# Kernel optimization log

Hardware: AMD Instinct MI355X
Metric: run time of the kernel (lower is better)

The kernel has to match this reference:

```python
import jax, jax.numpy as jnp
import numpy as np

DIM = 1024
N_OBJ = 2048
N_REL = 4096
H_CAT = 4
H_OUT = 6
OUT_CAT = DIM // 2            # 512, concat=True branch
OUT_NC = (DIM // 2) * H_OUT   # 3072, concat=False branch


def setup_inputs() -> dict:
    key = jax.random.key(0)
    ks = jax.random.split(key, 6)
    s = 0.02
    return {
        "feat_obj": jax.random.normal(ks[0], (N_OBJ, DIM), jnp.float32),
        "feat_rel": jax.random.normal(ks[1], (N_REL, DIM), jnp.float32),
        # 3 concat=True attentions, each with 4 Linears(dim -> dim/2)
        "W_cat": jax.random.normal(ks[2], (3, 4, DIM, OUT_CAT), jnp.float32) * s,
        "b_cat": jax.random.normal(ks[3], (3, 4, OUT_CAT), jnp.float32) * s,
        # 2 used concat=False attentions, each with 4 Linears(dim -> 6*dim/2)
        "W_out": jax.random.normal(ks[4], (2, 4, DIM, OUT_NC), jnp.float32) * s,
        "b_out": jax.random.normal(ks[5], (2, 4, OUT_NC), jnp.float32) * s,
    }


def _mha(xq, xk, Ws, bs, h, mask=None, concat=True):
    # Ws: [4, dim, out_dim], bs: [4, out_dim]
    out_dim = Ws.shape[-1]
    d_k = out_dim // h

    def proj(x, W, b):
        return (x @ W + b).reshape(-1, h, d_k).transpose(1, 0, 2)  # [h, N, d_k]

    q = proj(xq, Ws[0], bs[0])
    k = proj(xk, Ws[1], bs[1])
    qv = proj(xq, Ws[2], bs[2])
    kv = proj(xk, Ws[3], bs[3])
    scores = jnp.einsum('hnd,hmd->hnm', q, k) / jnp.sqrt(jnp.asarray(d_k, q.dtype))
    if mask is not None:
        scores = jnp.where(mask == 0, jnp.asarray(-1e9, scores.dtype), scores)
    p = jax.nn.softmax(scores, axis=-1)          # [h, Nq, Nk]
    a1 = jax.nn.elu(jnp.einsum('hnm,hmd->hnd', p, kv))  # per-head value mix (rows)
    a2 = jax.nn.elu(jnp.einsum('hnm,hnd->hmd', p, qv))  # transposed mix (cols)
    if concat:
        nq, nk = xq.shape[0], xk.shape[0]
        return a1.transpose(1, 0, 2).reshape(nq, out_dim), a2.transpose(1, 0, 2).reshape(nk, out_dim)
    return a1.sum(0), a2.sum(0)


def reference(feat_obj, feat_rel, W_cat, b_cat, W_out, b_out):
    n_obj = feat_obj.shape[0]
    mask = 1.0 - jnp.eye(n_obj, dtype=feat_obj.dtype)  # zero out self-attention

    sub_obj, obj_sub = _mha(feat_obj, feat_obj, W_cat[0], b_cat[0], H_CAT, mask, True)
    sub_rel, rel_sub = _mha(feat_obj, feat_rel, W_cat[1], b_cat[1], H_CAT, None, True)
    rel_obj, obj_rel = _mha(feat_rel, feat_obj, W_cat[2], b_cat[2], H_CAT, None, True)

    obj_feat = (feat_obj
                + jnp.concatenate((sub_obj, obj_sub), axis=1)
                + jnp.concatenate((sub_rel, obj_rel), axis=1)) / 3.0
    rel_feat = (feat_rel + jnp.concatenate((rel_obj, rel_sub), axis=1)) / 2.0

    _, rel_sub2 = _mha(obj_feat, rel_feat, W_out[0], b_out[0], H_OUT, None, False)
    rel_obj2, _ = _mha(rel_feat, obj_feat, W_out[1], b_out[1], H_OUT, None, False)
    rel_feat = (feat_rel + jnp.concatenate((rel_obj2, rel_sub2), axis=1)) / 2.0

    return obj_feat, rel_feat
```

## Files before the change

kernel.cpp:

```cpp
#include <hip/hip_runtime.h>

typedef unsigned short u16;
typedef unsigned int u32;
typedef __attribute__((ext_vector_type(4))) float f32x4;
typedef __attribute__((ext_vector_type(8))) __bf16 bf16x8;
typedef __attribute__((ext_vector_type(8))) unsigned short u16x8;

#if defined(__has_builtin)
#if __has_builtin(__builtin_amdgcn_global_load_lds)
#define HAS_GLL 1
#endif
#endif

__device__ __forceinline__ u16 f2bf(float f) {
    u32 u = __builtin_bit_cast(u32, f);
    u += 0x7fffu + ((u >> 16) & 1u);
    return (u16)(u >> 16);
}
__device__ __forceinline__ float bf2f(u16 x) {
    return __builtin_bit_cast(float, (u32)x << 16);
}

template <int N> __device__ __forceinline__ void wbar() {
#ifdef HAS_GLL
    if constexpr (N == 0)
        asm volatile("s_waitcnt vmcnt(0)\n\ts_barrier" ::: "memory");
    else if constexpr (N == 2)
        asm volatile("s_waitcnt vmcnt(2)\n\ts_barrier" ::: "memory");
    else
        asm volatile("s_waitcnt vmcnt(4)\n\ts_barrier" ::: "memory");
#else
    __syncthreads();
#endif
}

__device__ __forceinline__ void fbar() {
#ifdef HAS_GLL
    asm volatile("s_waitcnt vmcnt(0) lgkmcnt(0)\n\ts_barrier" ::: "memory");
#else
    __syncthreads();
#endif
}

__device__ __forceinline__ void rbar() {
#ifdef HAS_GLL
    asm volatile("s_barrier" ::: "memory");
#else
    __syncthreads();
#endif
}

__global__ __launch_bounds__(256) void zero_kernel(float* __restrict__ p, int n) {
    int i = blockIdx.x * 256 + threadIdx.x;
    if (i < n) p[i] = 0.f;
}

__global__ __launch_bounds__(256) void cvt_bf16_kernel(const float4* __restrict__ in,
                                                       ushort4* __restrict__ out, int n4) {
    int i = blockIdx.x * 256 + threadIdx.x;
    if (i < n4) {
        float4 v = in[i];
        ushort4 o;
        o.x = f2bf(v.x); o.y = f2bf(v.y); o.z = f2bf(v.z); o.w = f2bf(v.w);
        out[i] = o;
    }
}

__global__ __launch_bounds__(256) void transcvt_kernel(const float* __restrict__ W,
                                                       u16* __restrict__ Wt, int K, int N) {
    __shared__ u16 t[32][33];
    int b = blockIdx.z;
    const float* Wb = W + (size_t)b * K * N;
    u16* Wtb = Wt + (size_t)b * K * N;
    int n0 = blockIdx.x * 32, k0 = blockIdx.y * 32;
    int tx = threadIdx.x, ty = threadIdx.y;
#pragma unroll
    for (int j = 0; j < 4; ++j)
        t[ty + j * 8][tx] = f2bf(Wb[(size_t)(k0 + ty + j * 8) * N + n0 + tx]);
    __syncthreads();
#pragma unroll
    for (int j = 0; j < 4; ++j)
        Wtb[(size_t)(n0 + ty + j * 8) * K + k0 + tx] = t[tx][ty + j * 8];
}

__global__ __launch_bounds__(256) void scale_rows_kernel(const u16* __restrict__ in,
                                                         u16* __restrict__ out,
                                                         const float* __restrict__ rd,
                                                         int C, int lgdk) {
    int i = (blockIdx.x * 256 + threadIdx.x) * 8;
    int r = i / C, c = i % C;
    const float* rdp = rd + ((size_t)(r >> lgdk)) * C + c;
    u16x8 x = *reinterpret_cast<const u16x8*>(in + i);
    u16x8 o;
#pragma unroll
    for (int j = 0; j < 8; ++j) o[j] = f2bf(bf2f(x[j]) / rdp[j]);
    *reinterpret_cast<u16x8*>(out + i) = o;
}

struct FGrp { const u16* A; const u16* B; const u16* V; float* O; float* rs; int M; int NK; int mask; };
struct FCfg { FGrp g[3]; };

template <int NORM>
__global__ __launch_bounds__(256) void fused_attn1_kernel(FCfg cfg, float scale) {
    __shared__ __align__(16) u16 Abuf[4 * 2048];
    __shared__ __align__(16) u16 Bbuf[2][4 * 2048];
    __shared__ __align__(16) u16 Vbuf[2 * 4096];
    __shared__ __align__(16) u16 Pbuf[2 * 2048];
    __shared__ float rsum_lds[64][2];
    const int gi = blockIdx.z >> 2, h = blockIdx.z & 3;
    FGrp G = (gi == 0) ? cfg.g[0] : (gi == 1) ? cfg.g[1] : cfg.g[2];
    const int row0 = blockIdx.x * 64;
    if (row0 >= G.M) return;
    const u16* Ap = G.A + h * 128;
    const u16* Bp = G.B + h * 128;
    const u16* Vp = G.V + (size_t)h * 128 * G.NK;
    float* Op = G.O + h * 128;
    const int ldv = G.NK;
    const int tid = threadIdx.x, lane = tid & 63, wid = tid >> 6;
    const int swr = (wid >> 1) * 32, swc = (wid & 1) * 32;
    const int pwr = swr, pwc = (wid & 1) * 64;

    auto gld = [&](const u16* src, u16* dst) {
#ifdef HAS_GLL
        __builtin_amdgcn_global_load_lds(
            (const __attribute__((address_space(1))) void*)src,
            (__attribute__((address_space(3))) void*)dst, 16, 0, 0);
#else
        *reinterpret_cast<uint4*>(dst) = *reinterpret_cast<const uint4*>(src);
#endif
    };
    auto stageB = [&](int t, int buf) {
#pragma unroll
        for (int it = 0; it < 4; ++it) {
            int c = tid + it * 256;
            int kb = c >> 8, cc = c & 255;
            int r = cc >> 2, lch = (cc & 3) ^ ((r >> 1) & 3);
            gld(Bp + (size_t)(t * 64 + r) * 512 + kb * 32 + lch * 8, &Bbuf[buf][kb * 2048 + cc * 8]);
        }
    };
    auto stageV = [&](int t) {
#pragma unroll
        for (int it = 0; it < 4; ++it) {
            int c = tid + it * 256;
            int kb = c >> 9, cc = c & 511;
            int r = cc >> 2, lch = (cc & 3) ^ ((r >> 1) & 3);
            gld(Vp + (size_t)r * ldv + t * 64 + kb * 32 + lch * 8, &Vbuf[kb * 4096 + cc * 8]);
        }
    };

#pragma unroll
    for (int it = 0; it < 4; ++it) {
        int c = tid + it * 256;
        int kb = c >> 8, cc = c & 255;
        int r = cc >> 2, lch = (cc & 3) ^ ((r >> 1) & 3);
        gld(Ap + (size_t)(row0 + r) * 512 + kb * 32 + lch * 8, &Abuf[kb * 2048 + cc * 8]);
    }
    stageB(0, 0);
    stageB(1, 1);
    fbar();
    stageV(0);

    f32x4 accp[2][4] = {};
    float rsum[2][4] = {};
    const int nt = G.NK >> 6;
    for (int t = 0; t < nt; ++t) {
        const u16* Bc = &Bbuf[t & 1][0];
        f32x4 accs[2][2] = {};
#pragma unroll
        for (int kk = 0; kk < 4; ++kk) {
            bf16x8 af[2], bf[2];
#pragma unroll
            for (int m = 0; m < 2; ++m) {
                int rr = swr + m * 16 + (lane & 15);
                int p = (lane >> 4) ^ ((rr >> 1) & 3);
                af[m] = *reinterpret_cast<const bf16x8*>(&Abuf[kk * 2048 + rr * 32 + p * 8]);
            }
#pragma unroll
            for (int n = 0; n < 2; ++n) {
                int rr = swc + n * 16 + (lane & 15);
                int p = (lane >> 4) ^ ((rr >> 1) & 3);
                bf[n] = *reinterpret_cast<const bf16x8*>(&Bc[kk * 2048 + rr * 32 + p * 8]);
            }
#pragma unroll
            for (int m = 0; m < 2; ++m)
#pragma unroll
                for (int n = 0; n < 2; ++n)
                    accs[m][n] = __builtin_amdgcn_mfma_f32_16x16x32_bf16(af[m], bf[n], accs[m][n], 0, 0, 0);
        }
        float rsv[2];
        if (NORM == 0) {
#pragma unroll
            for (int n = 0; n < 2; ++n)
                rsv[n] = G.rs[(size_t)h * G.NK + t * 64 + swc + n * 16 + (lane & 15)];
        }
#pragma unroll
        for (int m = 0; m < 2; ++m) {
#pragma unroll
            for (int n = 0; n < 2; ++n) {
#pragma unroll
                for (int j = 0; j < 4; ++j) {
                    int prow = swr + m * 16 + ((lane >> 4) << 2) + j;
                    int pkey = swc + n * 16 + (lane & 15);
                    float v = __expf(accs[m][n][j] * scale);
                    if (NORM == 0) v *= rsv[n];
                    if (G.mask && (row0 + prow == t * 64 + pkey)) v = 0.f;
                    if (NORM == 1) rsum[m][j] += v;
                    Pbuf[(pkey >> 5) * 2048 + prow * 32 +
                         ((((pkey >> 3) & 3) ^ ((prow >> 1) & 3)) << 3) + (pkey & 7)] = f2bf(v);
                }
            }
        }
        fbar();
        if (t + 2 < nt) stageB(t + 2, t & 1);
#pragma unroll
        for (int kk = 0; kk < 2; ++kk) {
            bf16x8 pf[2], vf[4];
#pragma unroll
            for (int m = 0; m < 2; ++m) {
                int rr = pwr + m * 16 + (lane & 15);
                int p = (lane >> 4) ^ ((rr >> 1) & 3);
                pf[m] = *reinterpret_cast<const bf16x8*>(&Pbuf[kk * 2048 + rr * 32 + p * 8]);
            }
#pragma unroll
            for (int n = 0; n < 4; ++n) {
                int dd = pwc + n * 16 + (lane & 15);
                int p = (lane >> 4) ^ ((dd >> 1) & 3);
                vf[n] = *reinterpret_cast<const bf16x8*>(&Vbuf[kk * 4096 + dd * 32 + p * 8]);
            }
#pragma unroll
            for (int m = 0; m < 2; ++m)
#pragma unroll
                for (int n = 0; n < 4; ++n)
                    accp[m][n] = __builtin_amdgcn_mfma_f32_16x16x32_bf16(pf[m], vf[n], accp[m][n], 0, 0, 0);
        }
        rbar();
        if (t + 1 < nt) stageV(t + 1);
    }

    if (NORM == 1) {
#pragma unroll
        for (int m = 0; m < 2; ++m)
#pragma unroll
            for (int j = 0; j < 4; ++j) {
                float s = rsum[m][j];
                s += __shfl_xor(s, 1); s += __shfl_xor(s, 2);
                s += __shfl_xor(s, 4); s += __shfl_xor(s, 8);
                rsum[m][j] = s;
            }
        if ((lane & 15) == 0) {
#pragma unroll
            for (int m = 0; m < 2; ++m)
#pragma unroll
                for (int j = 0; j < 4; ++j)
                    rsum_lds[swr + m * 16 + ((lane >> 4) << 2) + j][wid & 1] = rsum[m][j];
        }
        __syncthreads();
        if (tid < 64)
            G.rs[(size_t)h * G.M + row0 + tid] = 1.f / (rsum_lds[tid][0] + rsum_lds[tid][1]);
#pragma unroll
        for (int m = 0; m < 2; ++m) {
#pragma unroll
            for (int j = 0; j < 4; ++j) {
                int row = pwr + m * 16 + ((lane >> 4) << 2) + j;
                float rd = 1.f / (rsum_lds[row][0] + rsum_lds[row][1]);
#pragma unroll
                for (int n = 0; n < 4; ++n) {
                    float v = accp[m][n][j] * rd;
                    v = v > 0.f ? v : (__expf(v) - 1.f);
                    Op[(size_t)(row0 + row) * 512 + pwc + n * 16 + (lane & 15)] = v;
                }
            }
        }
    } else {
#pragma unroll
        for (int m = 0; m < 2; ++m) {
#pragma unroll
            for (int j = 0; j < 4; ++j) {
                int row = pwr + m * 16 + ((lane >> 4) << 2) + j;
#pragma unroll
                for (int n = 0; n < 4; ++n) {
                    float v = accp[m][n][j];
                    v = v > 0.f ? v : (__expf(v) - 1.f);
                    Op[(size_t)(row0 + row) * 512 + pwc + n * 16 + (lane & 15)] = v;
                }
            }
        }
    }
}

enum { E_PROJ = 0, E_PROJT, E_EXP, E_EXPC, E_EXPT, E_EXPMT, E_PART };

template <int EPI, int BM>
__global__ __launch_bounds__(256) void gemm_nt(const u16* __restrict__ A, const u16* __restrict__ B,
                                               void* __restrict__ Cv, void* __restrict__ CvT,
                                               const float* __restrict__ bias, float* __restrict__ rs,
                                               int M, int N, int K, int lda, int ldb, int ldc, int ldcT,
                                               float scale, long sAz, long sBz, long sCz, long sCzT,
                                               long sBias, long sRs, int ZK, long sAz2, long sBz2) {
    constexpr bool HAS_BIAS = (EPI == E_PROJ || EPI == E_PROJT);
    constexpr bool DO_EXP = (EPI == E_EXP || EPI == E_EXPC || EPI == E_EXPT || EPI == E_EXPMT);
    constexpr bool DO_MASK = (EPI == E_EXPMT);
    constexpr int RSUM = (EPI == E_EXPC) ? 2 : (DO_EXP ? 1 : 0);
    constexpr bool STORE_N = (EPI != E_PROJT);
    constexpr bool STORE_T = (EPI == E_PROJT || EPI == E_EXPT || EPI == E_EXPMT);

    constexpr int MF = BM / 32;
    constexpr int ITERS = BM * 32 / (256 * 8);
    constexpr int LOADS = ITERS * 2;
    constexpr int SM_STAGE = 3 * BM * 64;
    constexpr int SM_REPACK = BM * BM;
    __shared__ __align__(16) u16 smem[SM_STAGE > SM_REPACK ? SM_STAGE : SM_REPACK];
    const int tid = threadIdx.x;
    const int lane = tid & 63;
    const int wid = tid >> 6;
    const int wr = (wid >> 1) * (BM / 2);
    const int wc = (wid & 1) * (BM / 2);
    const int row0 = blockIdx.x * BM;
    const int col0 = blockIdx.y * BM;
    const long zo = blockIdx.z;
    const long hz = zo / ZK;
    const long kz = zo - hz * ZK;
    const u16* Az = A + hz * sAz + kz * sAz2;
    const u16* Bz = B + hz * sBz + kz * sBz2;
    const float* biasz = bias ? bias + zo * sBias : nullptr;
    float* rsz = rs ? rs + zo * sRs : nullptr;
    f32x4 acc[MF][MF] = {};

    auto As = [&](int buf) { return smem + buf * (BM * 64); };
    auto Bs = [&](int buf) { return smem + buf * (BM * 64) + BM * 32; };

    auto stage = [&](int buf, int k0) {
#pragma unroll
        for (int i = 0; i < ITERS; ++i) {
            int c = tid + i * 256;
            int r = c >> 2;
            int lch = (c & 3) ^ ((r >> 1) & 3);
            const u16* sa = Az + (size_t)(row0 + r) * lda + k0 + lch * 8;
            const u16* sb = Bz + (size_t)(col0 + r) * ldb + k0 + lch * 8;
#ifdef HAS_GLL
            __builtin_amdgcn_global_load_lds(
                (const __attribute__((address_space(1))) void*)sa,
                (__attribute__((address_space(3))) void*)(&As(buf)[c * 8]), 16, 0, 0);
            __builtin_amdgcn_global_load_lds(
                (const __attribute__((address_space(1))) void*)sb,
                (__attribute__((address_space(3))) void*)(&Bs(buf)[c * 8]), 16, 0, 0);
#else
            *reinterpret_cast<uint4*>(&As(buf)[c * 8]) = *reinterpret_cast<const uint4*>(sa);
            *reinterpret_cast<uint4*>(&Bs(buf)[c * 8]) = *reinterpret_cast<const uint4*>(sb);
#endif
        }
    };

    stage(0, 0);
    stage(1, 32);
    wbar<LOADS>();

    const int nsteps = K >> 5;
    for (int t = 0; t < nsteps; ++t) {
        const int bufc = t % 3;
        const bool more2 = (t + 2 < nsteps);
        if (more2) stage((t + 2) % 3, (t + 2) << 5);
        bf16x8 af[MF], bv[MF];
#pragma unroll
        for (int m = 0; m < MF; ++m) {
            int rr = wr + m * 16 + (lane & 15);
            int p = (lane >> 4) ^ ((rr >> 1) & 3);
            af[m] = *reinterpret_cast<const bf16x8*>(&As(bufc)[rr * 32 + p * 8]);
        }
#pragma unroll
        for (int n = 0; n < MF; ++n) {
            int rr = wc + n * 16 + (lane & 15);
            int p = (lane >> 4) ^ ((rr >> 1) & 3);
            bv[n] = *reinterpret_cast<const bf16x8*>(&Bs(bufc)[rr * 32 + p * 8]);
        }
#pragma unroll
        for (int m = 0; m < MF; ++m)
#pragma unroll
            for (int n = 0; n < MF; ++n)
                acc[m][n] = __builtin_amdgcn_mfma_f32_16x16x32_bf16(af[m], bv[n], acc[m][n], 0, 0, 0);
        if (more2)                 wbar<LOADS>();
        else if (t + 1 < nsteps)   wbar<0>();
        else                       __syncthreads();
    }

#pragma unroll
    for (int m = 0; m < MF; ++m) {
#pragma unroll
        for (int n = 0; n < MF; ++n) {
#pragma unroll
            for (int j = 0; j < 4; ++j) {
                float v = acc[m][n][j];
                if (HAS_BIAS) v += biasz[col0 + wc + n * 16 + (lane & 15)];
                if (DO_EXP) {
                    v = __expf(v * scale);
                    if (DO_MASK &&
                        row0 + wr + m * 16 + ((lane >> 4) << 2) + j ==
                        col0 + wc + n * 16 + (lane & 15)) v = 0.f;
                }
                acc[m][n][j] = v;
            }
        }
    }

    if (RSUM == 1) {
#pragma unroll
        for (int m = 0; m < MF; ++m) {
#pragma unroll
            for (int j = 0; j < 4; ++j) {
                float p = 0.f;
#pragma unroll
                for (int n = 0; n < MF; ++n) p += acc[m][n][j];
                p += __shfl_xor(p, 1); p += __shfl_xor(p, 2);
                p += __shfl_xor(p, 4); p += __shfl_xor(p, 8);
                if ((lane & 15) == 0)
                    atomicAdd(rsz + row0 + wr + m * 16 + ((lane >> 4) << 2) + j, p);
            }
        }
    } else if (RSUM == 2) {
#pragma unroll
        for (int n = 0; n < MF; ++n) {
            float p = 0.f;
#pragma unroll
            for (int m = 0; m < MF; ++m)
#pragma unroll
                for (int j = 0; j < 4; ++j) p += acc[m][n][j];
            p += __shfl_xor(p, 16); p += __shfl_xor(p, 32);
            if (lane < 16) atomicAdd(rsz + col0 + wc + n * 16 + lane, p);
        }
    }

    char* lc = reinterpret_cast<char*>(smem);
    if (STORE_N) {
#pragma unroll
        for (int m = 0; m < MF; ++m) {
#pragma unroll
            for (int n = 0; n < MF; ++n) {
#pragma unroll
                for (int j = 0; j < 4; ++j) {
                    int lrow = wr + m * 16 + ((lane >> 4) << 2) + j;
                    int lcol = wc + n * 16 + (lane & 15);
                    u32 byte = (u32)((lrow * BM + lcol) * 2) ^ (((lrow >> 2) & 3) << 5);
                    *reinterpret_cast<u16*>(lc + byte) = f2bf(acc[m][n][j]);
                }
            }
        }
        __syncthreads();
        constexpr int CH = BM / 8;
        constexpr int NIT = BM * CH / 256;
        u16* Cp = reinterpret_cast<u16*>(Cv) + zo * sCz;
#pragma unroll
        for (int it = 0; it < NIT; ++it) {
            int idx = it * 256 + tid;
            int rrow = idx / CH, c8 = idx % CH;
            u32 byte = (u32)((rrow * BM + c8 * 8) * 2) ^ (((rrow >> 2) & 3) << 5);
            u16x8 val = *reinterpret_cast<const u16x8*>(lc + byte);
            *reinterpret_cast<u16x8*>(Cp + (size_t)(row0 + rrow) * ldc + col0 + c8 * 8) = val;
        }
    }
    if (STORE_T) {
        __syncthreads();
#pragma unroll
        for (int m = 0; m < MF; ++m) {
#pragma unroll
            for (int n = 0; n < MF; ++n) {
                int lcol = wc + n * 16 + (lane & 15);
                int lrow0 = wr + m * 16 + ((lane >> 4) << 2);
                u32 byte = (u32)((lcol * BM + lrow0) * 2) ^ ((u32)(lcol & 7) << 4);
                u32 lo = (u32)f2bf(acc[m][n][0]) | ((u32)f2bf(acc[m][n][1]) << 16);
                u32 hi = (u32)f2bf(acc[m][n][2]) | ((u32)f2bf(acc[m][n][3]) << 16);
                uint2 pk; pk.x = lo; pk.y = hi;
                *reinterpret_cast<uint2*>(lc + byte) = pk;
            }
        }
        __syncthreads();
        constexpr int CHT = BM / 8;
        constexpr int NITT = BM * CHT / 256;
        u16* Tp = reinterpret_cast<u16*>(CvT) + zo * sCzT;
#pragma unroll
        for (int it = 0; it < NITT; ++it) {
            int idx = it * 256 + tid;
            int c = idx / CHT, r8 = idx % CHT;
            u32 byte = (u32)((c * BM + r8 * 8) * 2) ^ ((u32)(c & 7) << 4);
            u16x8 val = *reinterpret_cast<const u16x8*>(lc + byte);
            *reinterpret_cast<u16x8*>(Tp + (size_t)(col0 + c) * ldcT + row0 + r8 * 8) = val;
        }
    }
}

__global__ __launch_bounds__(256) void reduce_h_elu_kernel(const u16* __restrict__ part,
                                                           float* __restrict__ out, int R, int H,
                                                           const float* __restrict__ rd) {
    int i = blockIdx.x * 256 + threadIdx.x;
    int row = i >> 6, c8 = i & 63;
    long plane = (long)R * 512;
    const u16* p = part + (size_t)row * 512 + c8 * 8;
    float s[8] = {};
    for (int h = 0; h < H; ++h) {
        u16x8 x = *reinterpret_cast<const u16x8*>(p + (size_t)h * plane);
        float r = rd ? 1.f / rd[(size_t)h * R + row] : 1.f;
#pragma unroll
        for (int j = 0; j < 8; ++j) {
            float v = bf2f(x[j]) * r;
            s[j] += v > 0.f ? v : (__expf(v) - 1.f);
        }
    }
    float4* o = reinterpret_cast<float4*>(out + (size_t)row * 512 + c8 * 8);
    o[0] = float4{s[0], s[1], s[2], s[3]};
    o[1] = float4{s[4], s[5], s[6], s[7]};
}

__global__ __launch_bounds__(256) void combine_obj_kernel(const float4* __restrict__ feat,
        const float4* __restrict__ a, const float4* __restrict__ b,
        const float4* __restrict__ c, const float4* __restrict__ d,
        float4* __restrict__ out, ushort4* __restrict__ outbf) {
    int i = blockIdx.x * 256 + threadIdx.x;
    int r = i >> 8, c4 = i & 255;
    size_t half = (size_t)r * 128 + (c4 & 127);
    float4 t1 = (c4 < 128) ? a[half] : b[half];
    float4 t2 = (c4 < 128) ? c[half] : d[half];
    float4 f = feat[i];
    float4 o;
    o.x = (f.x + t1.x + t2.x) * (1.f / 3.f);
    o.y = (f.y + t1.y + t2.y) * (1.f / 3.f);
    o.z = (f.z + t1.z + t2.z) * (1.f / 3.f);
    o.w = (f.w + t1.w + t2.w) * (1.f / 3.f);
    out[i] = o;
    ushort4 ob; ob.x = f2bf(o.x); ob.y = f2bf(o.y); ob.z = f2bf(o.z); ob.w = f2bf(o.w);
    outbf[i] = ob;
}

__global__ __launch_bounds__(256) void combine_rel1_kernel(const float4* __restrict__ feat,
        const float4* __restrict__ a, const float4* __restrict__ b, ushort4* __restrict__ outbf) {
    int i = blockIdx.x * 256 + threadIdx.x;
    int r = i >> 8, c4 = i & 255;
    size_t half = (size_t)r * 128 + (c4 & 127);
    float4 t = (c4 < 128) ? a[half] : b[half];
    float4 f = feat[i];
    ushort4 ob;
    ob.x = f2bf((f.x + t.x) * 0.5f); ob.y = f2bf((f.y + t.y) * 0.5f);
    ob.z = f2bf((f.z + t.z) * 0.5f); ob.w = f2bf((f.w + t.w) * 0.5f);
    outbf[i] = ob;
}

__global__ __launch_bounds__(256) void combine_rel2_kernel(const float4* __restrict__ feat,
        const float4* __restrict__ a, const float4* __restrict__ b, float4* __restrict__ out) {
    int i = blockIdx.x * 256 + threadIdx.x;
    int r = i >> 8, c4 = i & 255;
    size_t half = (size_t)r * 128 + (c4 & 127);
    float4 t = (c4 < 128) ? a[half] : b[half];
    float4 f = feat[i];
    float4 o;
    o.x = (f.x + t.x) * 0.5f; o.y = (f.y + t.y) * 0.5f;
    o.z = (f.z + t.z) * 0.5f; o.w = (f.w + t.w) * 0.5f;
    out[i] = o;
}

extern "C" void kernel_launch(void* const* d_in, const int* in_sizes, int n_in,
                              void* d_out, int out_size, void* d_ws, size_t ws_size,
                              hipStream_t stream) {
    (void)in_sizes; (void)n_in; (void)out_size; (void)ws_size;
    const float* feat_obj = (const float*)d_in[0];
    const float* feat_rel = (const float*)d_in[1];
    const float* W_cat = (const float*)d_in[2];
    const float* b_cat = (const float*)d_in[3];
    const float* W_out = (const float*)d_in[4];
    const float* b_out = (const float*)d_in[5];
    float* out_obj = (float*)d_out;
    float* out_rel = (float*)d_out + (size_t)2048 * 1024;

    char* w = (char*)d_ws;
    auto alloc = [&](size_t bytes) { void* p = (void*)w; w += (bytes + 255) & ~(size_t)255; return p; };
    u16* bf_obj  = (u16*)alloc((size_t)2048 * 1024 * 2);
    u16* bf_rel  = (u16*)alloc((size_t)4096 * 1024 * 2);
    u16* bf_obj2 = (u16*)alloc((size_t)2048 * 1024 * 2);
    u16* bf_rel2 = (u16*)alloc((size_t)4096 * 1024 * 2);
    u16* Wt_cat  = (u16*)alloc((size_t)12 * 512 * 1024 * 2);
    u16* Q01   = (u16*)alloc((size_t)2 * 2048 * 512 * 2);
    u16* K02   = (u16*)alloc((size_t)2 * 2048 * 512 * 2);
    u16* Q2    = (u16*)alloc((size_t)4096 * 512 * 2);
    u16* K1    = (u16*)alloc((size_t)4096 * 512 * 2);
    u16* Vq01T = (u16*)alloc((size_t)2 * 512 * 2048 * 2);
    u16* Vk02T = (u16*)alloc((size_t)2 * 512 * 2048 * 2);
    u16* Vk1T  = (u16*)alloc((size_t)512 * 4096 * 2);
    u16* Vq2T  = (u16*)alloc((size_t)512 * 4096 * 2);
    u16* Pq2   = (u16*)alloc((size_t)2 * 2048 * 3072 * 2);
    u16* Pk2   = (u16*)alloc((size_t)2 * 4096 * 3072 * 2);
    u16* VTa   = (u16*)alloc((size_t)2 * 3072 * 2048 * 2);
    u16* VTs   = (u16*)alloc((size_t)3072 * 2048 * 2);
    u16* Sbuf  = (u16*)alloc((size_t)6 * 4096 * 2048 * 2);
    u16* Wt2   = Sbuf;
    u16* part  = (u16*)alloc((size_t)6 * 4096 * 512 * 2);
    float* rdAll = (float*)alloc((size_t)36864 * 4);
    float* rdQ = rdAll;
    float* rdM = rdAll + 12288;
    float* rs0 = (float*)alloc((size_t)4 * 2048 * 4);
    float* rs1 = (float*)alloc((size_t)4 * 2048 * 4);
    float* rs2 = (float*)alloc((size_t)4 * 4096 * 4);
    float* sub_obj  = (float*)alloc((size_t)2048 * 512 * 4);
    float* obj_sub  = (float*)alloc((size_t)2048 * 512 * 4);
    float* sub_rel  = (float*)alloc((size_t)2048 * 512 * 4);
    float* obj_rel  = (float*)alloc((size_t)2048 * 512 * 4);
    float* rel_obj  = (float*)alloc((size_t)4096 * 512 * 4);
    float* rel_sub  = (float*)alloc((size_t)4096 * 512 * 4);
    float* rel_obj2 = (float*)alloc((size_t)4096 * 512 * 4);
    float* rel_sub2 = (float*)alloc((size_t)4096 * 512 * 4);

    zero_kernel<<<144, 256, 0, stream>>>(rdAll, 36864);
    cvt_bf16_kernel<<<2048, 256, 0, stream>>>((const float4*)feat_obj, (ushort4*)bf_obj, 2048 * 1024 / 4);
    cvt_bf16_kernel<<<4096, 256, 0, stream>>>((const float4*)feat_rel, (ushort4*)bf_rel, 4096 * 1024 / 4);
    transcvt_kernel<<<dim3(16, 32, 12), dim3(32, 8), 0, stream>>>(W_cat, Wt_cat, 1024, 512);
    transcvt_kernel<<<dim3(96, 32, 8), dim3(32, 8), 0, stream>>>(W_out, Wt2, 1024, 3072);

    const float sc1 = 0.08838834764831845f;
    const float sc2 = 0.04419417382415922f;
    const long planeW = (long)512 * 1024;
    const long planeW2 = (long)3072 * 1024;
    const long NIL = 0;

    gemm_nt<E_PROJ, 64><<<dim3(32, 8, 2), 256, 0, stream>>>(
        bf_obj, Wt_cat, Q01, nullptr, b_cat, nullptr,
        2048, 512, 1024, 1024, 1024, 512, 0, 0.f, NIL, 4 * planeW, (long)2048 * 512, NIL,
        4L * 512, NIL, 1, NIL, NIL);
    gemm_nt<E_PROJ, 64><<<dim3(32, 8, 2), 256, 0, stream>>>(
        bf_obj, Wt_cat + planeW, K02, nullptr, b_cat + 512, nullptr,
        2048, 512, 1024, 1024, 1024, 512, 0, 0.f, NIL, 8 * planeW, (long)2048 * 512, NIL,
        8L * 512, NIL, 1, NIL, NIL);
    gemm_nt<E_PROJT, 64><<<dim3(32, 8, 2), 256, 0, stream>>>(
        bf_obj, Wt_cat + 2 * planeW, nullptr, Vq01T, b_cat + 1024, nullptr,
        2048, 512, 1024, 1024, 1024, 0, 2048, 0.f, NIL, 4 * planeW, NIL, (long)512 * 2048,
        4L * 512, NIL, 1, NIL, NIL);
    gemm_nt<E_PROJT, 64><<<dim3(32, 8, 2), 256, 0, stream>>>(
        bf_obj, Wt_cat + 3 * planeW, nullptr, Vk02T, b_cat + 1536, nullptr,
        2048, 512, 1024, 1024, 1024, 0, 2048, 0.f, NIL, 8 * planeW, NIL, (long)512 * 2048,
        8L * 512, NIL, 1, NIL, NIL);
    gemm_nt<E_PROJ, 64><<<dim3(64, 8, 1), 256, 0, stream>>>(
        bf_rel, Wt_cat + 5 * planeW, K1, nullptr, b_cat + 5 * 512, nullptr,
        4096, 512, 1024, 1024, 1024, 512, 0, 0.f, NIL, NIL, NIL, NIL, NIL, NIL, 1, NIL, NIL);
    gemm_nt<E_PROJ, 64><<<dim3(64, 8, 1), 256, 0, stream>>>(
        bf_rel, Wt_cat + 8 * planeW, Q2, nullptr, b_cat + 8 * 512, nullptr,
        4096, 512, 1024, 1024, 1024, 512, 0, 0.f, NIL, NIL, NIL, NIL, NIL, NIL, 1, NIL, NIL);
    gemm_nt<E_PROJT, 64><<<dim3(64, 8, 1), 256, 0, stream>>>(
        bf_rel, Wt_cat + 7 * planeW, nullptr, Vk1T, b_cat + 7 * 512, nullptr,
        4096, 512, 1024, 1024, 1024, 0, 4096, 0.f, NIL, NIL, NIL, NIL, NIL, NIL, 1, NIL, NIL);
    gemm_nt<E_PROJT, 64><<<dim3(64, 8, 1), 256, 0, stream>>>(
        bf_rel, Wt_cat + 10 * planeW, nullptr, Vq2T, b_cat + 10 * 512, nullptr,
        4096, 512, 1024, 1024, 1024, 0, 4096, 0.f, NIL, NIL, NIL, NIL, NIL, NIL, 1, NIL, NIL);

    FCfg f1, f2;
    f1.g[0] = { Q01,                    K02,                    Vk02T,                    sub_obj, rs0, 2048, 2048, 1 };
    f1.g[1] = { Q01 + (size_t)2048*512, K1,                     Vk1T,                     sub_rel, rs1, 2048, 4096, 0 };
    f1.g[2] = { Q2,                     K02 + (size_t)2048*512, Vk02T + (size_t)512*2048, rel_obj, rs2, 4096, 2048, 0 };
    fused_attn1_kernel<1><<<dim3(64, 1, 12), 256, 0, stream>>>(f1, sc1);
    f2.g[0] = { K02,                    Q01,                    Vq01T,                    obj_sub, rs0, 2048, 2048, 1 };
    f2.g[1] = { K1,                     Q01 + (size_t)2048*512, Vq01T + (size_t)512*2048, rel_sub, rs1, 4096, 2048, 0 };
    f2.g[2] = { K02 + (size_t)2048*512, Q2,                     Vq2T,                     obj_rel, rs2, 2048, 4096, 0 };
    fused_attn1_kernel<0><<<dim3(64, 1, 12), 256, 0, stream>>>(f2, sc1);

    combine_obj_kernel<<<2048, 256, 0, stream>>>((const float4*)feat_obj, (const float4*)sub_obj,
        (const float4*)obj_sub, (const float4*)sub_rel, (const float4*)obj_rel,
        (float4*)out_obj, (ushort4*)bf_obj2);
    combine_rel1_kernel<<<4096, 256, 0, stream>>>((const float4*)feat_rel, (const float4*)rel_obj,
        (const float4*)rel_sub, (ushort4*)bf_rel2);

    gemm_nt<E_PROJ, 128><<<dim3(16, 24, 2), 256, 0, stream>>>(
        bf_obj2, Wt2, Pq2, nullptr, b_out, nullptr,
        2048, 3072, 1024, 1024, 1024, 3072, 0, 0.f, NIL, 5 * planeW2, (long)2048 * 3072, NIL,
        5L * 3072, NIL, 1, NIL, NIL);
    gemm_nt<E_PROJ, 128><<<dim3(32, 24, 2), 256, 0, stream>>>(
        bf_rel2, Wt2 + planeW2, Pk2, nullptr, b_out + 3072, nullptr,
        4096, 3072, 1024, 1024, 1024, 3072, 0, 0.f, NIL, 3 * planeW2, (long)4096 * 3072, NIL,
        3L * 3072, NIL, 1, NIL, NIL);
    gemm_nt<E_PROJT, 128><<<dim3(16, 24, 2), 256, 0, stream>>>(
        bf_obj2, Wt2 + 2 * planeW2, nullptr, VTa, b_out + 2 * 3072, nullptr,
        2048, 3072, 1024, 1024, 1024, 0, 2048, 0.f, NIL, 5 * planeW2, NIL, (long)3072 * 2048,
        5L * 3072, NIL, 1, NIL, NIL);

    const long spl2 = (long)4096 * 2048;
    const long vpl2 = (long)4096 * 512;

    {
        gemm_nt<E_EXPC, 128><<<dim3(32, 16, 6), 256, 0, stream>>>(
            Pk2, Pq2, Sbuf, nullptr, nullptr, rdQ,
            4096, 2048, 512, 3072, 3072, 2048, 0, sc2, 512, 512, spl2, NIL, NIL, 2048, 1, NIL, NIL);
        scale_rows_kernel<<<3072 * 2048 / 2048, 256, 0, stream>>>(VTa, VTs, rdQ, 2048, 9);
        gemm_nt<E_PART, 128><<<dim3(32, 4, 6), 256, 0, stream>>>(
            Sbuf, VTs, part, nullptr, nullptr, nullptr,
            4096, 512, 2048, 2048, 2048, 512, 0, 0.f, spl2, 512L * 2048, vpl2, NIL, NIL, NIL,
            1, NIL, NIL);
        reduce_h_elu_kernel<<<1024, 256, 0, stream>>>(part, rel_sub2, 4096, 6, nullptr);
    }
    {
        gemm_nt<E_EXP, 128><<<dim3(32, 16, 6), 256, 0, stream>>>(
            Pk2 + (size_t)4096 * 3072, Pq2 + (size_t)2048 * 3072, Sbuf, nullptr, nullptr, rdM,
            4096, 2048, 512, 3072, 3072, 2048, 0, sc2, 512, 512, spl2, NIL, NIL, 4096, 1, NIL, NIL);
        gemm_nt<E_PART, 128><<<dim3(32, 4, 6), 256, 0, stream>>>(
            Sbuf, VTa + (size_t)3072 * 2048, part, nullptr, nullptr, nullptr,
            4096, 512, 2048, 2048, 2048, 512, 0, 0.f, spl2, 512L * 2048, vpl2, NIL, NIL, NIL,
            1, NIL, NIL);
        reduce_h_elu_kernel<<<1024, 256, 0, stream>>>(part, rel_obj2, 4096, 6, rdM);
    }

    combine_rel2_kernel<<<4096, 256, 0, stream>>>((const float4*)feat_rel, (const float4*)rel_obj2,
        (const float4*)rel_sub2, (float4*)out_rel);
}
```

Measured before the change: 812.7 us.

## Double-buffer V tiles, keep Q fragments in registers, prescale V by row sums

The fused attention kernel now loads the A (query) fragments straight from global memory into registers instead of staging them in shared memory. It double-buffers the V tiles alongside the B tiles so the next V tile is prefetched two iterations ahead, with lighter barriers in the loop. The per-key row-sum scaling in the NORM=0 pass moves out of the inner loop into separate in-place scale_rows launches on the V matrices. This trades extra small kernel launches and an extra pass over V for fewer LDS reads and better overlap of global loads, at the cost of more registers per thread.

```diff
diff --git a/kernel.cpp b/kernel.cpp
--- a/kernel.cpp
+++ b/kernel.cpp
@@ -42,9 +42,9 @@
 #endif
 }
 
-__device__ __forceinline__ void rbar() {
+__device__ __forceinline__ void lbar() {
 #ifdef HAS_GLL
-    asm volatile("s_barrier" ::: "memory");
+    asm volatile("s_waitcnt lgkmcnt(0)\n\ts_barrier" ::: "memory");
 #else
     __syncthreads();
 #endif
@@ -86,14 +86,15 @@
 __global__ __launch_bounds__(256) void scale_rows_kernel(const u16* __restrict__ in,
                                                          u16* __restrict__ out,
                                                          const float* __restrict__ rd,
-                                                         int C, int lgdk) {
+                                                         int C, int lgdk, int mul) {
     int i = (blockIdx.x * 256 + threadIdx.x) * 8;
     int r = i / C, c = i % C;
     const float* rdp = rd + ((size_t)(r >> lgdk)) * C + c;
     u16x8 x = *reinterpret_cast<const u16x8*>(in + i);
     u16x8 o;
 #pragma unroll
-    for (int j = 0; j < 8; ++j) o[j] = f2bf(bf2f(x[j]) / rdp[j]);
+    for (int j = 0; j < 8; ++j)
+        o[j] = f2bf(mul ? bf2f(x[j]) * rdp[j] : bf2f(x[j]) / rdp[j]);
     *reinterpret_cast<u16x8*>(out + i) = o;
 }
 
@@ -102,9 +103,8 @@
 
 template <int NORM>
 __global__ __launch_bounds__(256) void fused_attn1_kernel(FCfg cfg, float scale) {
-    __shared__ __align__(16) u16 Abuf[4 * 2048];
     __shared__ __align__(16) u16 Bbuf[2][4 * 2048];
-    __shared__ __align__(16) u16 Vbuf[2 * 4096];
+    __shared__ __align__(16) u16 Vbuf[2][2 * 4096];
     __shared__ __align__(16) u16 Pbuf[2 * 2048];
     __shared__ float rsum_lds[64][2];
     const int gi = blockIdx.z >> 2, h = blockIdx.z & 3;
@@ -138,60 +138,51 @@
             gld(Bp + (size_t)(t * 64 + r) * 512 + kb * 32 + lch * 8, &Bbuf[buf][kb * 2048 + cc * 8]);
         }
     };
-    auto stageV = [&](int t) {
+    auto stageV = [&](int t, int buf) {
 #pragma unroll
         for (int it = 0; it < 4; ++it) {
             int c = tid + it * 256;
             int kb = c >> 9, cc = c & 511;
             int r = cc >> 2, lch = (cc & 3) ^ ((r >> 1) & 3);
-            gld(Vp + (size_t)r * ldv + t * 64 + kb * 32 + lch * 8, &Vbuf[kb * 4096 + cc * 8]);
+            gld(Vp + (size_t)r * ldv + t * 64 + kb * 32 + lch * 8, &Vbuf[buf][kb * 4096 + cc * 8]);
         }
     };
 
-#pragma unroll
-    for (int it = 0; it < 4; ++it) {
-        int c = tid + it * 256;
-        int kb = c >> 8, cc = c & 255;
-        int r = cc >> 2, lch = (cc & 3) ^ ((r >> 1) & 3);
-        gld(Ap + (size_t)(row0 + r) * 512 + kb * 32 + lch * 8, &Abuf[kb * 2048 + cc * 8]);
+    bf16x8 areg[2][4];
+#pragma unroll
+    for (int m = 0; m < 2; ++m) {
+        int rr = swr + m * 16 + (lane & 15);
+#pragma unroll
+        for (int kk = 0; kk < 4; ++kk)
+            areg[m][kk] = *reinterpret_cast<const bf16x8*>(
+                Ap + (size_t)(row0 + rr) * 512 + kk * 32 + (lane >> 4) * 8);
     }
     stageB(0, 0);
+    stageV(0, 0);
     stageB(1, 1);
+    stageV(1, 1);
     fbar();
-    stageV(0);
 
     f32x4 accp[2][4] = {};
     float rsum[2][4] = {};
     const int nt = G.NK >> 6;
     for (int t = 0; t < nt; ++t) {
-        const u16* Bc = &Bbuf[t & 1][0];
+        const int cur = t & 1;
         f32x4 accs[2][2] = {};
 #pragma unroll
         for (int kk = 0; kk < 4; ++kk) {
-            bf16x8 af[2], bf[2];
-#pragma unroll
-            for (int m = 0; m < 2; ++m) {
-                int rr = swr + m * 16 + (lane & 15);
-                int p = (lane >> 4) ^ ((rr >> 1) & 3);
-                af[m] = *reinterpret_cast<const bf16x8*>(&Abuf[kk * 2048 + rr * 32 + p * 8]);
-            }
+            bf16x8 bf[2];
 #pragma unroll
             for (int n = 0; n < 2; ++n) {
                 int rr = swc + n * 16 + (lane & 15);
                 int p = (lane >> 4) ^ ((rr >> 1) & 3);
-                bf[n] = *reinterpret_cast<const bf16x8*>(&Bc[kk * 2048 + rr * 32 + p * 8]);
+                bf[n] = *reinterpret_cast<const bf16x8*>(&Bbuf[cur][kk * 2048 + rr * 32 + p * 8]);
             }
 #pragma unroll
             for (int m = 0; m < 2; ++m)
 #pragma unroll
                 for (int n = 0; n < 2; ++n)
-                    accs[m][n] = __builtin_amdgcn_mfma_f32_16x16x32_bf16(af[m], bf[n], accs[m][n], 0, 0, 0);
-        }
-        float rsv[2];
-        if (NORM == 0) {
-#pragma unroll
-            for (int n = 0; n < 2; ++n)
-                rsv[n] = G.rs[(size_t)h * G.NK + t * 64 + swc + n * 16 + (lane & 15)];
+                    accs[m][n] = __builtin_amdgcn_mfma_f32_16x16x32_bf16(areg[m][kk], bf[n], accs[m][n], 0, 0, 0);
         }
 #pragma unroll
         for (int m = 0; m < 2; ++m) {
@@ -202,7 +193,6 @@
                     int prow = swr + m * 16 + ((lane >> 4) << 2) + j;
                     int pkey = swc + n * 16 + (lane & 15);
                     float v = __expf(accs[m][n][j] * scale);
-                    if (NORM == 0) v *= rsv[n];
                     if (G.mask && (row0 + prow == t * 64 + pkey)) v = 0.f;
                     if (NORM == 1) rsum[m][j] += v;
                     Pbuf[(pkey >> 5) * 2048 + prow * 32 +
@@ -210,8 +200,8 @@
                 }
             }
         }
-        fbar();
-        if (t + 2 < nt) stageB(t + 2, t & 1);
+        lbar();
+        if (t + 2 < nt) stageB(t + 2, cur);
 #pragma unroll
         for (int kk = 0; kk < 2; ++kk) {
             bf16x8 pf[2], vf[4];
@@ -225,7 +215,7 @@
             for (int n = 0; n < 4; ++n) {
                 int dd = pwc + n * 16 + (lane & 15);
                 int p = (lane >> 4) ^ ((dd >> 1) & 3);
-                vf[n] = *reinterpret_cast<const bf16x8*>(&Vbuf[kk * 4096 + dd * 32 + p * 8]);
+                vf[n] = *reinterpret_cast<const bf16x8*>(&Vbuf[cur][kk * 4096 + dd * 32 + p * 8]);
             }
 #pragma unroll
             for (int m = 0; m < 2; ++m)
@@ -233,8 +223,9 @@
                 for (int n = 0; n < 4; ++n)
                     accp[m][n] = __builtin_amdgcn_mfma_f32_16x16x32_bf16(pf[m], vf[n], accp[m][n], 0, 0, 0);
         }
-        rbar();
-        if (t + 1 < nt) stageV(t + 1);
+        if (t + 2 < nt)      wbar<4>();
+        else if (t + 1 < nt) wbar<0>();
+        if (t + 2 < nt) stageV(t + 2, cur);
     }
 
     if (NORM == 1) {
@@ -651,6 +642,9 @@
     f1.g[1] = { Q01 + (size_t)2048*512, K1,                     Vk1T,                     sub_rel, rs1, 2048, 4096, 0 };
     f1.g[2] = { Q2,                     K02 + (size_t)2048*512, Vk02T + (size_t)512*2048, rel_obj, rs2, 4096, 2048, 0 };
     fused_attn1_kernel<1><<<dim3(64, 1, 12), 256, 0, stream>>>(f1, sc1);
+    scale_rows_kernel<<<512, 256, 0, stream>>>(Vq01T, Vq01T, rs0, 2048, 7, 1);
+    scale_rows_kernel<<<512, 256, 0, stream>>>(Vq01T + (size_t)512 * 2048, Vq01T + (size_t)512 * 2048, rs1, 2048, 7, 1);
+    scale_rows_kernel<<<1024, 256, 0, stream>>>(Vq2T, Vq2T, rs2, 4096, 7, 1);
     f2.g[0] = { K02,                    Q01,                    Vq01T,                    obj_sub, rs0, 2048, 2048, 1 };
     f2.g[1] = { K1,                     Q01 + (size_t)2048*512, Vq01T + (size_t)512*2048, rel_sub, rs1, 4096, 2048, 0 };
     f2.g[2] = { K02 + (size_t)2048*512, Q2,                     Vq2T,                     obj_rel, rs2, 2048, 4096, 0 };
@@ -682,7 +676,7 @@
         gemm_nt<E_EXPC, 128><<<dim3(32, 16, 6), 256, 0, stream>>>(
             Pk2, Pq2, Sbuf, nullptr, nullptr, rdQ,
             4096, 2048, 512, 3072, 3072, 2048, 0, sc2, 512, 512, spl2, NIL, NIL, 2048, 1, NIL, NIL);
-        scale_rows_kernel<<<3072 * 2048 / 2048, 256, 0, stream>>>(VTa, VTs, rdQ, 2048, 9);
+        scale_rows_kernel<<<3072, 256, 0, stream>>>(VTa, VTs, rdQ, 2048, 9, 0);
         gemm_nt<E_PART, 128><<<dim3(32, 4, 6), 256, 0, stream>>>(
             Sbuf, VTs, part, nullptr, nullptr, nullptr,
             4096, 512, 2048, 2048, 2048, 512, 0, 0.f, spl2, 512L * 2048, vpl2, NIL, NIL, NIL,
```

Measured after the change: 818.1 us. Within noise of the previous version (+0.7%).
